# Kernel tuning notes

Hardware: AMD Instinct MI355X
Metric: run time of the kernel (lower is better)

Reference implementation:

```python
import jax, jax.numpy as jnp
import numpy as np

B, N, D = 8, 2048, 512
H = 8
DH = D // H          # 64
SR = 2               # sr_ratio
EPS = 1e-5


def setup_inputs() -> dict:
    key = jax.random.key(0)
    ks = jax.random.split(key, 10)
    s = 0.02
    return {
        "x": jax.random.normal(ks[0], (B, N, D), jnp.float32),
        "x_kv": jax.random.normal(ks[1], (B, N, D), jnp.float32),
        "Wq": jax.random.normal(ks[2], (D, D), jnp.float32) * s,
        "bq": jnp.zeros((D,), jnp.float32),
        "Wsr": jax.random.normal(ks[3], (D, D, SR), jnp.float32) * s,  # (out_ch, in_ch, kernel)
        "bsr": jnp.zeros((D,), jnp.float32),
        "gamma": jnp.ones((D,), jnp.float32),
        "beta": jnp.zeros((D,), jnp.float32),
        "Wkv": jax.random.normal(ks[4], (D, 2 * D), jnp.float32) * s,
        "bkv": jnp.zeros((2 * D,), jnp.float32),
        "Wp": jax.random.normal(ks[5], (DH, DH), jnp.float32) * s,
        "bp": jnp.zeros((DH,), jnp.float32),
    }


def reference(x, x_kv, Wq, bq, Wsr, bsr, gamma, beta, Wkv, bkv, Wp, bp):
    b, n, d = x.shape
    # query projection -> (B, N, H, DH)
    q = (x @ Wq + bq).reshape(b, n, H, DH)

    # spatial reduction: Conv1d(kernel=stride=SR) over sequence, then LayerNorm
    # non-overlapping windows -> reshape + einsum
    xk = x_kv.reshape(b, -1, SR, d)                      # (B, Nk/SR, SR, D)
    xk = jnp.einsum('btsi,ois->bto', xk, Wsr) + bsr       # (B, Nk_eff, D)
    mu = xk.mean(-1, keepdims=True)
    var = jnp.mean((xk - mu) ** 2, -1, keepdims=True)
    xk = (xk - mu) * jax.lax.rsqrt(var + EPS) * gamma + beta

    # kv projection: (B, Nk, 2, H, DH) -> (2, B, H, Nk, DH)
    nk = xk.shape[1]
    kv = (xk @ Wkv + bkv).reshape(b, nk, 2, H, DH)
    kv = jnp.transpose(kv, (2, 0, 3, 1, 4))
    k, v = kv[0], kv[1]                                   # (B, H, Nk, DH)

    # faithful reproduction of original permutes/views
    q = jnp.transpose(q, (2, 0, 1, 3)).reshape(b * H, n, DH)      # (H,B,N,d)->(BH,N,d)
    k = jnp.transpose(k, (2, 0, 1, 3)).reshape(b * H, nk, DH)     # (Nk,B,H,d)->(BH,Nk,d)
    v = jnp.transpose(v, (2, 0, 1, 3)).reshape(b * H, nk, DH)

    scale = float(np.sqrt(DH))
    score = jnp.einsum('bnd,bmd->bnm', q, k) / scale
    attn = jax.nn.softmax(score, axis=-1)
    ctx = jnp.einsum('bnm,bmd->bnd', attn, v)
    ctx = ctx @ Wp + bp                                   # per-head proj Linear(DH, DH)

    ctx = ctx.reshape(H, b, n, DH)
    ctx = jnp.transpose(ctx, (1, 2, 0, 3)).reshape(b, n, H * DH)
    return ctx, attn
```

## Files before the change

### kernel.cpp

```cpp
#include <hip/hip_runtime.h>
#include <cstdint>

using f32x4 = __attribute__((ext_vector_type(4))) float;
using s16x8 = __attribute__((ext_vector_type(8))) short;

__device__ __forceinline__ short f2bf(float f) {
    union { float f; uint32_t u; } x{f};
    uint32_t r = (x.u + 0x7fffu + ((x.u >> 16) & 1u)) >> 16;
    return (short)r;
}
__device__ __forceinline__ float bf2f(short s) {
    union { uint32_t u; float f; } x;
    x.u = ((uint32_t)(uint16_t)s) << 16;
    return x.f;
}

#define MFMA16(a, b, c) __builtin_amdgcn_mfma_f32_16x16x32_bf16(a, b, c, 0, 0, 0)

__device__ __forceinline__ void bar_lgkm() {
    asm volatile("s_waitcnt lgkmcnt(0)\n\ts_barrier" ::: "memory");
}

__device__ __forceinline__ void gl_lds16(const void* g, void* l) {
    __builtin_amdgcn_global_load_lds(
        (const __attribute__((address_space(1))) void*)(const void*)g,
        (__attribute__((address_space(3))) void*)l, 16, 0, 0);
}

__global__ __launch_bounds__(256) void prep_all(
    const float* __restrict__ Wq, const float* __restrict__ Wsr,
    const float* __restrict__ Wkv, const float* __restrict__ Wp,
    short* __restrict__ WqT, short* __restrict__ W2T,
    short* __restrict__ WkvT, short* __restrict__ WpT)
{
    const int b = blockIdx.x, tid = threadIdx.x;
    if (b < 192) {
        const float* src; short* dst; int K, N, tk, tn;
        if (b < 64) { src = Wq;  dst = WqT;  K = 512; N = 512;  tk = b >> 3; tn = b & 7; }
        else { int u = b - 64; src = Wkv; dst = WkvT; K = 512; N = 1024; tk = u >> 4; tn = u & 15; }
        const int k0 = tk * 64, n0 = tn * 64;
        __shared__ float t[64][65];
        const int lr = tid >> 2, lc = (tid & 3) * 16;
        const float* s = src + (size_t)(k0 + lr) * N + n0 + lc;
        float4 a0 = *(const float4*)s, a1 = *(const float4*)(s + 4);
        float4 a2 = *(const float4*)(s + 8), a3 = *(const float4*)(s + 12);
        *(float4*)&t[lr][lc]      = a0; *(float4*)&t[lr][lc + 4]  = a1;
        *(float4*)&t[lr][lc + 8]  = a2; *(float4*)&t[lr][lc + 12] = a3;
        __syncthreads();
        const int wn = tid >> 2, wk = (tid & 3) * 16;
        s16x8 o0, o1;
#pragma unroll
        for (int j = 0; j < 8; ++j) {
            o0[j] = f2bf(t[wk + j][wn]);
            o1[j] = f2bf(t[wk + 8 + j][wn]);
        }
        short* d = dst + (size_t)(n0 + wn) * K + k0 + wk;
        *(s16x8*)d = o0;
        *(s16x8*)(d + 8) = o1;
    } else {
        for (int u = (b - 192) * 256 + tid; u < 524288 + 4096; u += 208 * 256) {
            if (u < 524288) {
                int o = u >> 10, kk = u & 1023;
                int s2 = kk >> 9, i = kk & 511;
                W2T[u] = f2bf(Wsr[o * 1024 + i * 2 + s2]);
            } else {
                int v = u - 524288;
                int e = v >> 6, dh = v & 63;
                WpT[v] = f2bf(Wp[dh * 64 + e]);
            }
        }
    }
}

__global__ __launch_bounds__(256) void ln_kernel(
    const float* __restrict__ xkf, const float* __restrict__ gamma,
    const float* __restrict__ beta, short* __restrict__ out)
{
    int row = blockIdx.x * 4 + (threadIdx.x >> 6);
    int lane = threadIdx.x & 63;
    const float* p = xkf + (size_t)row * 512 + lane * 8;
    float4 v0 = *(const float4*)p, v1 = *(const float4*)(p + 4);
    float vv[8] = {v0.x, v0.y, v0.z, v0.w, v1.x, v1.y, v1.z, v1.w};
    float s = 0.f, q = 0.f;
#pragma unroll
    for (int j = 0; j < 8; ++j) { s += vv[j]; q += vv[j] * vv[j]; }
#pragma unroll
    for (int m = 1; m < 64; m <<= 1) { s += __shfl_xor(s, m); q += __shfl_xor(q, m); }
    float mean = s * (1.f / 512.f);
    float var  = q * (1.f / 512.f) - mean * mean;
    float rstd = rsqrtf(var + 1e-5f);
    s16x8 o;
#pragma unroll
    for (int j = 0; j < 8; ++j)
        o[j] = f2bf((vv[j] - mean) * rstd * gamma[lane * 8 + j] + beta[lane * 8 + j]);
    *(s16x8*)(out + (size_t)row * 512 + lane * 8) = o;
}

__global__ __launch_bounds__(256) void gemm_qconv(
    const float* __restrict__ x, const float* __restrict__ xkv,
    const short* __restrict__ WqT, const short* __restrict__ W2T,
    const float* __restrict__ bq, const float* __restrict__ bsr,
    short* __restrict__ Qb, float* __restrict__ xkf)
{
    __shared__ short As[128 * 32];
    __shared__ short Bs[128 * 32];
    const int tid = threadIdx.x;
    const int wv = tid >> 6, lane = tid & 63;
    const int l15 = lane & 15, lhi = lane >> 4;
    const int wr = wv >> 1, wc = wv & 1;

    const int bid = blockIdx.x;
    const int u0 = (bid & 7) * 96 + (bid >> 3);
    const bool isQ = u0 < 512;
    const int u = isQ ? u0 : u0 - 512;
    const int m0 = (u >> 2) * 128, n0 = (u & 3) * 128;
    const int K = isQ ? 512 : 1024;
    const float* A = isQ ? x : xkv;
    const short* BT = isQ ? WqT : W2T;
    const float* bias = isQ ? bq : bsr;

    f32x4 acc[4][4] = {};

    const int nk = K >> 5;
    for (int kk = 0; kk < nk; ++kk) {
#pragma unroll
        for (int i = 0; i < 2; ++i) {
            int fo = wv * 2048 + i * 1024 + lane * 16;
            int row = fo >> 6;
            int ks  = (fo & 63) >> 1;
            const float* src = A + (size_t)(m0 + row) * K + kk * 32 + ks;
            float4 a0 = *(const float4*)src;
            float4 a1 = *(const float4*)(src + 4);
            s16x8 pk;
            pk[0] = f2bf(a0.x); pk[1] = f2bf(a0.y); pk[2] = f2bf(a0.z); pk[3] = f2bf(a0.w);
            pk[4] = f2bf(a1.x); pk[5] = f2bf(a1.y); pk[6] = f2bf(a1.z); pk[7] = f2bf(a1.w);
            *(s16x8*)((char*)As + fo) = pk;
            gl_lds16(BT + (size_t)(n0 + row) * K + kk * 32 + ks, (char*)Bs + fo);
        }
        __syncthreads();
        s16x8 a[4], b[4];
#pragma unroll
        for (int mi = 0; mi < 4; ++mi)
            a[mi] = *(const s16x8*)&As[(wr * 64 + mi * 16 + l15) * 32 + lhi * 8];
#pragma unroll
        for (int ni = 0; ni < 4; ++ni)
            b[ni] = *(const s16x8*)&Bs[(wc * 64 + ni * 16 + l15) * 32 + lhi * 8];
#pragma unroll
        for (int mi = 0; mi < 4; ++mi)
#pragma unroll
            for (int ni = 0; ni < 4; ++ni)
                acc[mi][ni] = MFMA16(a[mi], b[ni], acc[mi][ni]);
        __syncthreads();
    }

#pragma unroll
    for (int mi = 0; mi < 4; ++mi) {
#pragma unroll
        for (int ni = 0; ni < 4; ++ni) {
#pragma unroll
            for (int r = 0; r < 4; ++r) {
                int grow = m0 + wr * 64 + mi * 16 + lhi * 4 + r;
                int gcol = n0 + wc * 64 + ni * 16 + l15;
                float v = acc[mi][ni][r] + bias[gcol];
                if (isQ) {
                    int h = gcol >> 6, dh = gcol & 63;
                    int bb = grow >> 11, n = grow & 2047;
                    Qb[(((size_t)(h * 8 + bb) * 2048 + n) << 6) + dh] = f2bf(v * 0.18033688f);
                } else {
                    xkf[(size_t)grow * 512 + gcol] = v;
                }
            }
        }
    }
}

__global__ __launch_bounds__(256) void gemm_kv(
    const short* __restrict__ A, const short* __restrict__ BT,
    const float* __restrict__ bias,
    short* __restrict__ Kb, short* __restrict__ VTb)
{
    __shared__ short As[128 * 32];
    __shared__ short Bs[128 * 32];
    const int tid = threadIdx.x;
    const int wv = tid >> 6, lane = tid & 63;
    const int l15 = lane & 15, lhi = lane >> 4;
    const int wr = wv >> 1, wc = wv & 1;
    const int K = 512;
    const int u = (blockIdx.x & 7) * 64 + (blockIdx.x >> 3);
    const int m0 = (u >> 3) * 128, n0 = (u & 7) * 128;

    f32x4 acc[4][4] = {};

    const int nk = K >> 5;
    for (int kk = 0; kk < nk; ++kk) {
#pragma unroll
        for (int i = 0; i < 2; ++i) {
            int fo = wv * 2048 + i * 1024 + lane * 16;
            int row = fo >> 6;
            int ks  = (fo & 63) >> 1;
            gl_lds16(A + (size_t)(m0 + row) * K + kk * 32 + ks, (char*)As + fo);
            gl_lds16(BT + (size_t)(n0 + row) * K + kk * 32 + ks, (char*)Bs + fo);
        }
        __syncthreads();
        s16x8 a[4], b[4];
#pragma unroll
        for (int mi = 0; mi < 4; ++mi)
            a[mi] = *(const s16x8*)&As[(wr * 64 + mi * 16 + l15) * 32 + lhi * 8];
#pragma unroll
        for (int ni = 0; ni < 4; ++ni)
            b[ni] = *(const s16x8*)&Bs[(wc * 64 + ni * 16 + l15) * 32 + lhi * 8];
#pragma unroll
        for (int mi = 0; mi < 4; ++mi)
#pragma unroll
            for (int ni = 0; ni < 4; ++ni)
                acc[mi][ni] = MFMA16(a[mi], b[ni], acc[mi][ni]);
        __syncthreads();
    }

#pragma unroll
    for (int mi = 0; mi < 4; ++mi) {
#pragma unroll
        for (int ni = 0; ni < 4; ++ni) {
#pragma unroll
            for (int r = 0; r < 4; ++r) {
                int grow = m0 + wr * 64 + mi * 16 + lhi * 4 + r;
                int gcol = n0 + wc * 64 + ni * 16 + l15;
                float v = acc[mi][ni][r] + bias[gcol];
                int kvsel = gcol >> 9, h = (gcol >> 6) & 7, dh = gcol & 63;
                int bb = grow >> 10, t = grow & 1023;
                int g2 = t >> 4, m = ((t & 15) << 6) + bb * 8 + h;
                if (kvsel == 0)
                    Kb[(((size_t)g2 * 1024 + m) << 6) + dh] = f2bf(v);
                else
                    VTb[(((size_t)g2 * 64 + dh) << 10) + m] = f2bf(v);
            }
        }
    }
}

__global__ __launch_bounds__(512, 4) void attn_kernel(
    const short* __restrict__ Qb, const short* __restrict__ Kb,
    const short* __restrict__ VTb, const short* __restrict__ WpT,
    const float* __restrict__ bp,
    float* __restrict__ ctx_out, float* __restrict__ attn_out)
{
    __shared__ __align__(16) char smem[65536];
    __shared__ float sums[8][32];

    const int bid = blockIdx.x;
    const int swz = ((bid & 7) << 9) | (bid >> 3);
    const int g  = swz >> 6;
    const int n0 = (swz & 63) << 5;
    const int tid = threadIdx.x;
    const int wv = tid >> 6, lane = tid & 63;
    const int l15 = lane & 15, lhi = lane >> 4;

    s16x8 qa00, qa01, qa10, qa11;
    {
        size_t qb0 = (((size_t)g * 2048 + n0 + l15) << 6) + lhi * 8;
        size_t qb1 = (((size_t)g * 2048 + n0 + 16 + l15) << 6) + lhi * 8;
        qa00 = *(const s16x8*)&Qb[qb0];
        qa01 = *(const s16x8*)&Qb[qb0 + 32];
        qa10 = *(const s16x8*)&Qb[qb1];
        qa11 = *(const s16x8*)&Qb[qb1 + 32];
    }

    const short* Kg = Kb + ((size_t)g << 16);
    s16x8 kf[4][2];
#pragma unroll
    for (int p = 0; p < 4; ++p) {
        const short* kr = Kg + (((wv * 8 + p) * 16 + l15) << 6) + lhi * 8;
        kf[p][0] = *(const s16x8*)kr;
        kf[p][1] = *(const s16x8*)(kr + 32);
    }
    float ps0[4] = {}, ps1[4] = {};
#pragma unroll
    for (int i = 0; i < 8; ++i) {
        s16x8 k0 = kf[i & 3][0], k1 = kf[i & 3][1];
        if (i < 4) {
            const short* kr = Kg + (((wv * 8 + i + 4) * 16 + l15) << 6) + lhi * 8;
            kf[i][0] = *(const s16x8*)kr;
            kf[i][1] = *(const s16x8*)(kr + 32);
        }
        int mf = wv * 8 + i;
        f32x4 s0 = {0.f, 0.f, 0.f, 0.f};
        s0 = MFMA16(qa00, k0, s0);
        s0 = MFMA16(qa01, k1, s0);
        f32x4 s1 = {0.f, 0.f, 0.f, 0.f};
        s1 = MFMA16(qa10, k0, s1);
        s1 = MFMA16(qa11, k1, s1);
#pragma unroll
        for (int r = 0; r < 4; ++r) {
            float e0 = exp2f(s0[r]);
            ps0[r] += e0;
            int row0 = lhi * 4 + r;
            int byte0 = ((row0 << 11) + ((mf * 16 + l15) << 1)) ^ ((row0 & 7) << 4);
            *(short*)(smem + byte0) = f2bf(e0);
            float e1 = exp2f(s1[r]);
            ps1[r] += e1;
            int row1 = 16 + lhi * 4 + r;
            int byte1 = ((row1 << 11) + ((mf * 16 + l15) << 1)) ^ ((row1 & 7) << 4);
            *(short*)(smem + byte1) = f2bf(e1);
        }
    }

    const short* Vg = VTb + ((size_t)g << 16);
    s16x8 vb[2][4];
#pragma unroll
    for (int ni = 0; ni < 4; ++ni) {
        vb[0][ni] = *(const s16x8*)&Vg[((ni * 16 + l15) << 10) + wv * 128 + lhi * 8];
        vb[1][ni] = *(const s16x8*)&Vg[((ni * 16 + l15) << 10) + wv * 128 + 32 + lhi * 8];
    }

#pragma unroll
    for (int r = 0; r < 4; ++r) {
        float v0 = ps0[r], v1 = ps1[r];
        v0 += __shfl_xor(v0, 1); v1 += __shfl_xor(v1, 1);
        v0 += __shfl_xor(v0, 2); v1 += __shfl_xor(v1, 2);
        v0 += __shfl_xor(v0, 4); v1 += __shfl_xor(v1, 4);
        v0 += __shfl_xor(v0, 8); v1 += __shfl_xor(v1, 8);
        ps0[r] = v0; ps1[r] = v1;
    }
    if (l15 == 0) {
#pragma unroll
        for (int r = 0; r < 4; ++r) {
            sums[wv][lhi * 4 + r] = ps0[r];
            sums[wv][16 + lhi * 4 + r] = ps1[r];
        }
    }
    bar_lgkm();

#pragma unroll
    for (int rr = 0; rr < 4; ++rr) {
        int row = wv * 4 + rr;
        float tot = 0.f;
#pragma unroll
        for (int w = 0; w < 8; ++w) tot += sums[w][row];
        float inv = 1.f / tot;
        float* arow = attn_out + (((size_t)g * 2048 + n0 + row) << 10);
#pragma unroll
        for (int it = 0; it < 2; ++it) {
            int col = it * 512 + lane * 8;
            int byte = ((row << 11) + (col << 1)) ^ ((row & 7) << 4);
            s16x8 p = *(const s16x8*)(smem + byte);
            f32x4 w0 = {bf2f(p[0]) * inv, bf2f(p[1]) * inv, bf2f(p[2]) * inv, bf2f(p[3]) * inv};
            f32x4 w1 = {bf2f(p[4]) * inv, bf2f(p[5]) * inv, bf2f(p[6]) * inv, bf2f(p[7]) * inv};
            __builtin_nontemporal_store(w0, (f32x4*)(arow + col));
            __builtin_nontemporal_store(w1, (f32x4*)(arow + col + 4));
        }
    }

    f32x4 ctx0[4] = {}, ctx1[4] = {};
#pragma unroll
    for (int kk = 0; kk < 4; ++kk) {
        int col = wv * 128 + kk * 32 + lhi * 8;
        s16x8 pv[4];
#pragma unroll
        for (int ni = 0; ni < 4; ++ni) pv[ni] = vb[kk & 1][ni];
        if (kk < 2) {
            int ncol = wv * 128 + (kk + 2) * 32 + lhi * 8;
#pragma unroll
            for (int ni = 0; ni < 4; ++ni)
                vb[kk][ni] = *(const s16x8*)&Vg[((ni * 16 + l15) << 10) + ncol];
        }
        int b0 = ((l15 << 11) + (col << 1)) ^ ((l15 & 7) << 4);
        int b1 = (((16 + l15) << 11) + (col << 1)) ^ ((l15 & 7) << 4);
        s16x8 pf0 = *(const s16x8*)(smem + b0);
        s16x8 pf1 = *(const s16x8*)(smem + b1);
#pragma unroll
        for (int ni = 0; ni < 4; ++ni) {
            ctx0[ni] = MFMA16(pf0, pv[ni], ctx0[ni]);
            ctx1[ni] = MFMA16(pf1, pv[ni], ctx1[ni]);
        }
    }

    bar_lgkm();
    float* cx = (float*)smem;
    if (wv >= 4) {
        int q = wv - 4;
#pragma unroll
        for (int ni = 0; ni < 4; ++ni)
#pragma unroll
            for (int r = 0; r < 4; ++r) {
                cx[(q * 32 + lhi * 4 + r) * 68 + ni * 16 + l15] = ctx0[ni][r];
                cx[(q * 32 + 16 + lhi * 4 + r) * 68 + ni * 16 + l15] = ctx1[ni][r];
            }
    }
    bar_lgkm();
    if (wv < 4) {
#pragma unroll
        for (int ni = 0; ni < 4; ++ni)
#pragma unroll
            for (int r = 0; r < 4; ++r) {
                cx[(wv * 32 + lhi * 4 + r) * 68 + ni * 16 + l15] += ctx0[ni][r];
                cx[(wv * 32 + 16 + lhi * 4 + r) * 68 + ni * 16 + l15] += ctx1[ni][r];
            }
    }
    bar_lgkm();

    if (wv < 2) {
        int rbase = wv * 16;
        float tot = 0.f;
#pragma unroll
        for (int w = 0; w < 8; ++w) tot += sums[w][rbase + l15];
        float invq = 1.f / tot;
        s16x8 ca[2];
#pragma unroll
        for (int kk = 0; kk < 2; ++kk)
#pragma unroll
            for (int j = 0; j < 8; ++j) {
                int k = kk * 32 + lhi * 8 + j;
                int ri = (rbase + l15) * 68 + k;
                float v = cx[ri] + cx[2176 + ri] + cx[4352 + ri] + cx[6528 + ri];
                ca[kk][j] = f2bf(v * invq);
            }
        f32x4 acc2[4] = {};
#pragma unroll
        for (int ni = 0; ni < 4; ++ni) {
            s16x8 b0 = *(const s16x8*)&WpT[((ni * 16 + l15) << 6) + lhi * 8];
            s16x8 b1 = *(const s16x8*)&WpT[((ni * 16 + l15) << 6) + 32 + lhi * 8];
            acc2[ni] = MFMA16(ca[0], b0, acc2[ni]);
            acc2[ni] = MFMA16(ca[1], b1, acc2[ni]);
        }
        const int hh = g >> 3, bb = g & 7;
#pragma unroll
        for (int ni = 0; ni < 4; ++ni)
#pragma unroll
            for (int r = 0; r < 4; ++r) {
                int n = n0 + rbase + lhi * 4 + r;
                int e2 = ni * 16 + l15;
                float ov = acc2[ni][r] + bp[e2];
                __builtin_nontemporal_store(
                    ov, ctx_out + ((size_t)bb * 2048 + n) * 512 + hh * 64 + e2);
            }
    }
}

extern "C" void kernel_launch(void* const* d_in, const int* in_sizes, int n_in,
                              void* d_out, int out_size, void* d_ws, size_t ws_size,
                              hipStream_t stream)
{
    const float* x     = (const float*)d_in[0];
    const float* xkv   = (const float*)d_in[1];
    const float* Wq    = (const float*)d_in[2];
    const float* bq    = (const float*)d_in[3];
    const float* Wsr   = (const float*)d_in[4];
    const float* bsr   = (const float*)d_in[5];
    const float* gamma = (const float*)d_in[6];
    const float* beta  = (const float*)d_in[7];
    const float* Wkv   = (const float*)d_in[8];
    const float* bkv   = (const float*)d_in[9];
    const float* Wp    = (const float*)d_in[10];
    const float* bp    = (const float*)d_in[11];

    float* ctx_out  = (float*)d_out;
    float* attn_out = ctx_out + (size_t)8 * 2048 * 512;

    char* sc = (char*)attn_out;
    float* xkf  = (float*)sc;  sc += (size_t)8192 * 512 * 4;
    short* xkln = (short*)sc;  sc += (size_t)8192 * 512 * 2;
    short* WqT  = (short*)sc;  sc += (size_t)512 * 512 * 2;
    short* W2T  = (short*)sc;  sc += (size_t)512 * 1024 * 2;
    short* WkvT = (short*)sc;  sc += (size_t)1024 * 512 * 2;

    char* ws = (char*)d_ws;
    short* Qb  = (short*)ws;   ws += (size_t)64 * 2048 * 64 * 2;
    short* Kb  = (short*)ws;   ws += (size_t)64 * 1024 * 64 * 2;
    short* VTb = (short*)ws;   ws += (size_t)64 * 64 * 1024 * 2;
    short* WpT = (short*)ws;   ws += (size_t)64 * 64 * 2;

    prep_all<<<400, 256, 0, stream>>>(Wq, Wsr, Wkv, Wp, WqT, W2T, WkvT, WpT);
    gemm_qconv<<<768, 256, 0, stream>>>(x, xkv, WqT, W2T, bq, bsr, Qb, xkf);
    ln_kernel<<<2048, 256, 0, stream>>>(xkf, gamma, beta, xkln);
    gemm_kv<<<512, 256, 0, stream>>>(xkln, WkvT, bkv, Kb, VTb);
    attn_kernel<<<4096, 512, 0, stream>>>(Qb, Kb, VTb, WpT, bp, ctx_out, attn_out);
}
```

Measured before the change: 290.8 us.

## Fuse LayerNorm into conv GEMM epilogue stats and KV GEMM prologue

Removes the standalone LayerNorm kernel. The conv GEMM epilogue now accumulates per-row sum and sum-of-squares with atomics into a zeroed buffer, and the KV GEMM normalizes fp32 rows while staging its A tile into LDS. This saves one launch and the bf16 intermediate round trip. In exchange, the KV GEMM reads fp32 A (twice the bytes), loses async global-to-LDS loads for A, and recomputes normalization for every N tile. It also adds a memset and atomic traffic.

```diff
diff --git a/kernel.cpp b/kernel.cpp
--- a/kernel.cpp
+++ b/kernel.cpp
@@ -72,35 +72,12 @@
     }
 }
 
-__global__ __launch_bounds__(256) void ln_kernel(
-    const float* __restrict__ xkf, const float* __restrict__ gamma,
-    const float* __restrict__ beta, short* __restrict__ out)
-{
-    int row = blockIdx.x * 4 + (threadIdx.x >> 6);
-    int lane = threadIdx.x & 63;
-    const float* p = xkf + (size_t)row * 512 + lane * 8;
-    float4 v0 = *(const float4*)p, v1 = *(const float4*)(p + 4);
-    float vv[8] = {v0.x, v0.y, v0.z, v0.w, v1.x, v1.y, v1.z, v1.w};
-    float s = 0.f, q = 0.f;
-#pragma unroll
-    for (int j = 0; j < 8; ++j) { s += vv[j]; q += vv[j] * vv[j]; }
-#pragma unroll
-    for (int m = 1; m < 64; m <<= 1) { s += __shfl_xor(s, m); q += __shfl_xor(q, m); }
-    float mean = s * (1.f / 512.f);
-    float var  = q * (1.f / 512.f) - mean * mean;
-    float rstd = rsqrtf(var + 1e-5f);
-    s16x8 o;
-#pragma unroll
-    for (int j = 0; j < 8; ++j)
-        o[j] = f2bf((vv[j] - mean) * rstd * gamma[lane * 8 + j] + beta[lane * 8 + j]);
-    *(s16x8*)(out + (size_t)row * 512 + lane * 8) = o;
-}
-
 __global__ __launch_bounds__(256) void gemm_qconv(
     const float* __restrict__ x, const float* __restrict__ xkv,
     const short* __restrict__ WqT, const short* __restrict__ W2T,
     const float* __restrict__ bq, const float* __restrict__ bsr,
-    short* __restrict__ Qb, float* __restrict__ xkf)
+    short* __restrict__ Qb, float* __restrict__ xkf,
+    float* __restrict__ ssum, float* __restrict__ ssq)
 {
     __shared__ short As[128 * 32];
     __shared__ short Bs[128 * 32];
@@ -153,29 +130,51 @@
         __syncthreads();
     }
 
-#pragma unroll
-    for (int mi = 0; mi < 4; ++mi) {
-#pragma unroll
-        for (int ni = 0; ni < 4; ++ni) {
-#pragma unroll
-            for (int r = 0; r < 4; ++r) {
-                int grow = m0 + wr * 64 + mi * 16 + lhi * 4 + r;
-                int gcol = n0 + wc * 64 + ni * 16 + l15;
-                float v = acc[mi][ni][r] + bias[gcol];
-                if (isQ) {
+    if (isQ) {
+#pragma unroll
+        for (int mi = 0; mi < 4; ++mi)
+#pragma unroll
+            for (int ni = 0; ni < 4; ++ni)
+#pragma unroll
+                for (int r = 0; r < 4; ++r) {
+                    int grow = m0 + wr * 64 + mi * 16 + lhi * 4 + r;
+                    int gcol = n0 + wc * 64 + ni * 16 + l15;
+                    float v = acc[mi][ni][r] + bias[gcol];
                     int h = gcol >> 6, dh = gcol & 63;
                     int bb = grow >> 11, n = grow & 2047;
                     Qb[(((size_t)(h * 8 + bb) * 2048 + n) << 6) + dh] = f2bf(v * 0.18033688f);
-                } else {
+                }
+    } else {
+#pragma unroll
+        for (int mi = 0; mi < 4; ++mi) {
+#pragma unroll
+            for (int r = 0; r < 4; ++r) {
+                int grow = m0 + wr * 64 + mi * 16 + lhi * 4 + r;
+                float s = 0.f, q = 0.f;
+#pragma unroll
+                for (int ni = 0; ni < 4; ++ni) {
+                    int gcol = n0 + wc * 64 + ni * 16 + l15;
+                    float v = acc[mi][ni][r] + bias[gcol];
                     xkf[(size_t)grow * 512 + gcol] = v;
+                    s += v; q += v * v;
                 }
+                s += __shfl_xor(s, 1); q += __shfl_xor(q, 1);
+                s += __shfl_xor(s, 2); q += __shfl_xor(q, 2);
+                s += __shfl_xor(s, 4); q += __shfl_xor(q, 4);
+                s += __shfl_xor(s, 8); q += __shfl_xor(q, 8);
+                if (l15 == 0) {
+                    atomicAdd(&ssum[grow], s);
+                    atomicAdd(&ssq[grow], q);
+                }
             }
         }
     }
 }
 
 __global__ __launch_bounds__(256) void gemm_kv(
-    const short* __restrict__ A, const short* __restrict__ BT,
+    const float* __restrict__ xkf, const short* __restrict__ BT,
+    const float* __restrict__ ssum, const float* __restrict__ ssq,
+    const float* __restrict__ gamma, const float* __restrict__ beta,
     const float* __restrict__ bias,
     short* __restrict__ Kb, short* __restrict__ VTb)
 {
@@ -198,7 +197,27 @@
             int fo = wv * 2048 + i * 1024 + lane * 16;
             int row = fo >> 6;
             int ks  = (fo & 63) >> 1;
-            gl_lds16(A + (size_t)(m0 + row) * K + kk * 32 + ks, (char*)As + fo);
+            const int arow = m0 + row;
+            const float* src = xkf + (size_t)arow * 512 + kk * 32 + ks;
+            float4 a0 = *(const float4*)src;
+            float4 a1 = *(const float4*)(src + 4);
+            float mean = ssum[arow] * (1.f / 512.f);
+            float var  = ssq[arow] * (1.f / 512.f) - mean * mean;
+            float rstd = rsqrtf(var + 1e-5f);
+            const float* gp = gamma + kk * 32 + ks;
+            const float* bp = beta  + kk * 32 + ks;
+            float4 g0 = *(const float4*)gp, g1 = *(const float4*)(gp + 4);
+            float4 e0 = *(const float4*)bp, e1 = *(const float4*)(bp + 4);
+            s16x8 pk;
+            pk[0] = f2bf((a0.x - mean) * rstd * g0.x + e0.x);
+            pk[1] = f2bf((a0.y - mean) * rstd * g0.y + e0.y);
+            pk[2] = f2bf((a0.z - mean) * rstd * g0.z + e0.z);
+            pk[3] = f2bf((a0.w - mean) * rstd * g0.w + e0.w);
+            pk[4] = f2bf((a1.x - mean) * rstd * g1.x + e1.x);
+            pk[5] = f2bf((a1.y - mean) * rstd * g1.y + e1.y);
+            pk[6] = f2bf((a1.z - mean) * rstd * g1.z + e1.z);
+            pk[7] = f2bf((a1.w - mean) * rstd * g1.w + e1.w);
+            *(s16x8*)((char*)As + fo) = pk;
             gl_lds16(BT + (size_t)(n0 + row) * K + kk * 32 + ks, (char*)Bs + fo);
         }
         __syncthreads();
@@ -458,7 +477,6 @@
 
     char* sc = (char*)attn_out;
     float* xkf  = (float*)sc;  sc += (size_t)8192 * 512 * 4;
-    short* xkln = (short*)sc;  sc += (size_t)8192 * 512 * 2;
     short* WqT  = (short*)sc;  sc += (size_t)512 * 512 * 2;
     short* W2T  = (short*)sc;  sc += (size_t)512 * 1024 * 2;
     short* WkvT = (short*)sc;  sc += (size_t)1024 * 512 * 2;
@@ -468,10 +486,12 @@
     short* Kb  = (short*)ws;   ws += (size_t)64 * 1024 * 64 * 2;
     short* VTb = (short*)ws;   ws += (size_t)64 * 64 * 1024 * 2;
     short* WpT = (short*)ws;   ws += (size_t)64 * 64 * 2;
-
+    float* ssum = (float*)ws;  ws += (size_t)8192 * 4;
+    float* ssq  = (float*)ws;  ws += (size_t)8192 * 4;
+
+    hipMemsetAsync(ssum, 0, 2 * 8192 * sizeof(float), stream);
     prep_all<<<400, 256, 0, stream>>>(Wq, Wsr, Wkv, Wp, WqT, W2T, WkvT, WpT);
-    gemm_qconv<<<768, 256, 0, stream>>>(x, xkv, WqT, W2T, bq, bsr, Qb, xkf);
-    ln_kernel<<<2048, 256, 0, stream>>>(xkf, gamma, beta, xkln);
-    gemm_kv<<<512, 256, 0, stream>>>(xkln, WkvT, bkv, Kb, VTb);
+    gemm_qconv<<<768, 256, 0, stream>>>(x, xkv, WqT, W2T, bq, bsr, Qb, xkf, ssum, ssq);
+    gemm_kv<<<512, 256, 0, stream>>>(xkf, WkvT, ssum, ssq, gamma, beta, bkv, Kb, VTb);
     attn_kernel<<<4096, 512, 0, stream>>>(Qb, Kb, VTb, WpT, bp, ctx_out, attn_out);
 }
```

Result: slower. 300.7 us (+3.4%).
